# Kernel optimization log

Measured on AMD Instinct MI355X. Metric: run time of the kernel, lower is better.

The kernel has to match this reference:

```python
import jax, jax.numpy as jnp
import numpy as np

HID = 64
L = 3
RHO = 0.3
KMIN = 64
EPS = 1e-5


def conv1x1(x, w, b):
    # x: [B,C,H,W], w: [O,C], b: [O]
    return jnp.einsum('bchw,oc->bohw', x, w) + b[None, :, None, None]


def dwconv(x, w, pad, dil):
    # depthwise conv, w: [C,1,k,k], groups = C, no bias
    return jax.lax.conv_general_dilated(
        x, w, window_strides=(1, 1), padding=[(pad, pad), (pad, pad)],
        rhs_dilation=(dil, dil), feature_group_count=x.shape[1],
        dimension_numbers=('NCHW', 'OIHW', 'NCHW'))


def conv3x3(x, w, b):
    return jax.lax.conv_general_dilated(
        x, w, (1, 1), [(1, 1), (1, 1)],
        dimension_numbers=('NCHW', 'OIHW', 'NCHW')) + b[None, :, None, None]


def bn(x, g, b):
    # training-mode BatchNorm2d: batch statistics over (B,H,W) per channel
    mu = jnp.mean(x, axis=(0, 2, 3), keepdims=True)
    var = jnp.var(x, axis=(0, 2, 3), keepdims=True)
    return g[None, :, None, None] * (x - mu) * jax.lax.rsqrt(var + EPS) + b[None, :, None, None]


def setup_inputs() -> dict:
    key = jax.random.key(0)
    ks = jax.random.split(key, 40)
    B, C, H, W = 8, 1, 224, 224
    d = {}
    d['x'] = jax.random.normal(ks[0], (B, C, H, W), jnp.float32)
    # input_proj: 1x1 conv, out = 2*HID + L + 1 = 132
    d['w_in'] = jax.random.normal(ks[1], (2 * HID + L + 1, C), jnp.float32) * 0.5
    d['b_in'] = jnp.zeros((2 * HID + L + 1,), jnp.float32)
    for l in range(L):
        ksz = 2 * l + 3
        d[f'dw{l}'] = jax.random.normal(ks[2 + 4 * l], (HID, 1, ksz, ksz), jnp.float32) / ksz
        d[f'pw{l}_w'] = jax.random.normal(ks[3 + 4 * l], (HID, HID), jnp.float32) * (1.0 / np.sqrt(HID))
        d[f'pw{l}_b'] = jnp.zeros((HID,), jnp.float32)
        d[f'bn{l}_g'] = jnp.ones((HID,), jnp.float32)
        d[f'bn{l}_b'] = jnp.zeros((HID,), jnp.float32)
    d['imp_w1'] = jax.random.normal(ks[20], (HID // 4, HID), jnp.float32) * (1.0 / np.sqrt(HID))
    d['imp_b1'] = jnp.zeros((HID // 4,), jnp.float32)
    d['imp_w2'] = jax.random.normal(ks[21], (1, HID // 4, 3, 3), jnp.float32) * 0.1
    d['imp_b2'] = jnp.zeros((1,), jnp.float32)
    d['val_w'] = jax.random.normal(ks[22], (HID, HID), jnp.float32) * (1.0 / np.sqrt(HID))
    d['val_b'] = jnp.zeros((HID,), jnp.float32)
    d['out_w'] = jax.random.normal(ks[23], (HID, HID), jnp.float32) * (1.0 / np.sqrt(HID))
    d['out_b'] = jnp.zeros((HID,), jnp.float32)
    d['fin_w'] = jax.random.normal(ks[24], (HID, HID), jnp.float32) * (1.0 / np.sqrt(HID))
    d['fin_b'] = jnp.zeros((HID,), jnp.float32)
    return d


def reference(x, w_in, b_in,
              dw0, pw0_w, pw0_b, bn0_g, bn0_b,
              dw1, pw1_w, pw1_b, bn1_g, bn1_b,
              dw2, pw2_w, pw2_b, bn2_g, bn2_b,
              imp_w1, imp_b1, imp_w2, imp_b2,
              val_w, val_b, out_w, out_b, fin_w, fin_b):
    B, C, H, W = x.shape
    F_ = conv1x1(x, w_in, b_in)                       # [B, 2*HID+L+1, H, W]
    Q = F_[:, :HID]
    K = F_[:, HID:2 * HID]
    G = F_[:, 2 * HID:]                               # [B, L+1, H, W]
    # importance network: 1x1 conv -> ReLU -> 3x3 conv -> sigmoid
    imp = jax.nn.sigmoid(conv3x3(jax.nn.relu(conv1x1(K, imp_w1, imp_b1)), imp_w2, imp_b2))  # [B,1,H,W]
    # adaptive top-k sparsification: K = max(floor(rho*H*W), K_min)
    k = max(int(RHO * H * W), KMIN)
    mask_flat = imp.reshape(B, H * W)
    _, idx = jax.lax.top_k(mask_flat, k)              # [B, k]
    sparse = jnp.zeros_like(mask_flat).at[jnp.arange(B)[:, None], idx].set(1.0)
    K_cur = K * sparse.reshape(B, 1, H, W)
    # focal levels: kernel k_l = 2*l+3, dilation d_l = 2^l, pad = (k_l//2)*d_l
    levels = [(dw0, pw0_w, pw0_b, bn0_g, bn0_b, 1),
              (dw1, pw1_w, pw1_b, bn1_g, bn1_b, 2),
              (dw2, pw2_w, pw2_b, bn2_g, bn2_b, 4)]
    focal = []
    for dw, pw_w, pw_b, g, be, dil in levels:
        ksz = dw.shape[-1]
        pad = (ksz // 2) * dil
        K_cur = jax.nn.relu(bn(conv1x1(dwconv(K_cur, dw, pad, dil), pw_w, pw_b), g, be))
        focal.append(K_cur)
    Gn = jax.nn.softmax(G, axis=1)                    # softmax over L+1 gate channels
    K_agg = Gn[:, 0:1] * focal[0] + Gn[:, 1:2] * focal[1] + Gn[:, 2:3] * focal[2]
    K_global = jnp.mean(focal[-1], axis=(2, 3), keepdims=True)  # AdaptiveAvgPool2d(1), broadcast
    K_final = K_agg + Gn[:, -1:] * K_global
    V = conv1x1(K_final, val_w, val_b)
    QV = Q * V
    # output_proj Linear over channel dim (dropout is identity in eval)
    O = jnp.einsum('bchw,oc->bohw', QV, out_w) + out_b[None, :, None, None]
    # in_channels (1) != hidden_channels -> residual via final_conv on F[:, :HID] == Q
    x_proj = conv1x1(Q, fin_w, fin_b)
    return x_proj + O
```

## Files before the change

kernel.cpp:

```cpp
#include <hip/hip_runtime.h>

#define HDIM 224
#define WDIM 224
#define PPIX 50176
#define BATCH 8
#define NPIX 401408
#define KTOP 15052
#define NELEM 25690112
#define NBLK 6272
#define NBAND 14
#define NDWBLK 7168
#define NCHUNK 49

typedef __attribute__((ext_vector_type(8))) short bf8_t;
typedef __attribute__((ext_vector_type(4))) float f4_t;
typedef __attribute__((ext_vector_type(8))) unsigned short us8_t;
typedef __attribute__((ext_vector_type(4))) unsigned short us4_t;
#define MFMA_BF16 __builtin_amdgcn_mfma_f32_16x16x32_bf16

__device__ inline unsigned short f2bf(float f) {
    unsigned int u = __float_as_uint(f);
    return (unsigned short)((u + 0x7FFFu + ((u >> 16) & 1u)) >> 16);
}
__device__ inline float bf2f(unsigned short u) {
    return __uint_as_float(((unsigned int)u) << 16);
}

__device__ inline int ldsg(int r) { return ((r >> 3) ^ r) & 7; }

__device__ inline void stage_w64(const float* __restrict__ W, char* sWc, int t) {
    int o = t >> 2, cq = t & 3, c0 = cq * 16;
    const float4* src = (const float4*)(W + o * 64 + c0);
    float4 v0 = src[0], v1 = src[1], v2 = src[2], v3 = src[3];
    bf8_t p0, p1;
    p0[0] = (short)f2bf(v0.x); p0[1] = (short)f2bf(v0.y);
    p0[2] = (short)f2bf(v0.z); p0[3] = (short)f2bf(v0.w);
    p0[4] = (short)f2bf(v1.x); p0[5] = (short)f2bf(v1.y);
    p0[6] = (short)f2bf(v1.z); p0[7] = (short)f2bf(v1.w);
    p1[0] = (short)f2bf(v2.x); p1[1] = (short)f2bf(v2.y);
    p1[2] = (short)f2bf(v2.z); p1[3] = (short)f2bf(v2.w);
    p1[4] = (short)f2bf(v3.x); p1[5] = (short)f2bf(v3.y);
    p1[6] = (short)f2bf(v3.z); p1[7] = (short)f2bf(v3.w);
    int g = ldsg(o);
    *(bf8_t*)(sWc + o * 128 + (((2 * cq) ^ g) << 4)) = p0;
    *(bf8_t*)(sWc + o * 128 + (((2 * cq + 1) ^ g) << 4)) = p1;
}

__device__ inline void mfma64(const char* sWc, const char* sPc, int l, int m0, f4_t acc[4]) {
    int lr = l & 15, lg = l >> 4;
    int ra = m0 + lr, ga = ldsg(ra);
    const char* abase = sWc + ra * 128;
    bf8_t a0 = *(const bf8_t*)(abase + ((lg ^ ga) << 4));
    bf8_t a1 = *(const bf8_t*)(abase + (((lg + 4) ^ ga) << 4));
    #pragma unroll
    for (int nt = 0; nt < 4; nt++) {
        int rb = nt * 16 + lr, gb = ldsg(rb);
        const char* bbase = sPc + rb * 128;
        bf8_t b0 = *(const bf8_t*)(bbase + ((lg ^ gb) << 4));
        bf8_t b1 = *(const bf8_t*)(bbase + (((lg + 4) ^ gb) << 4));
        f4_t c = {0.f, 0.f, 0.f, 0.f};
        c = MFMA_BF16(a0, b0, c, 0, 0, 0);
        c = MFMA_BF16(a1, b1, c, 0, 0, 0);
        acc[nt] = c;
    }
}

__global__ __launch_bounds__(256) void prep_kernel(
    const float* __restrict__ w_in, const float* __restrict__ b_in,
    const float* __restrict__ imp_w1, const float* __restrict__ imp_b1,
    const float* __restrict__ fin_w, const float* __restrict__ fin_b,
    float* __restrict__ coeffs, unsigned int* __restrict__ ghist,
    unsigned int* __restrict__ pfx, int* __restrict__ rem)
{
    int t = threadIdx.x;
    if (t < 16) {
        float a = 0.f, d = 0.f;
        for (int c = 0; c < 64; c++) {
            a += imp_w1[t * 64 + c] * w_in[64 + c];
            d += imp_w1[t * 64 + c] * b_in[64 + c];
        }
        coeffs[t] = a;
        coeffs[16 + t] = d + imp_b1[t];
    }
    if (t < 64) {
        float a = 0.f, d = 0.f;
        for (int c = 0; c < 64; c++) {
            a += fin_w[t * 64 + c] * w_in[c];
            d += fin_w[t * 64 + c] * b_in[c];
        }
        coeffs[32 + t] = a;
        coeffs[96 + t] = d + fin_b[t];
    }
    for (int i = t; i < 2048; i += 256) ghist[i] = 0u;
    if (t < BATCH) { pfx[t] = 0u; rem[t] = KTOP; }
}

__global__ __launch_bounds__(256) void imp_kernel(
    const float* __restrict__ x, const float* __restrict__ coeffs,
    const float* __restrict__ imp_w2, const float* __restrict__ imp_b2,
    float* __restrict__ imp)
{
    int idx = blockIdx.x * 256 + threadIdx.x;
    int b = idx / PPIX, p = idx % PPIX;
    int h = p / WDIM, w = p % WDIM;
    float acc = imp_b2[0];
    #pragma unroll
    for (int ky = 0; ky < 3; ky++) {
        int hh = h + ky - 1;
        float okh = (hh >= 0 && hh < HDIM) ? 1.f : 0.f;
        int hc = min(max(hh, 0), HDIM - 1);
        #pragma unroll
        for (int kx = 0; kx < 3; kx++) {
            int ww = w + kx - 1;
            float ok = okh * ((ww >= 0 && ww < WDIM) ? 1.f : 0.f);
            int wc = min(max(ww, 0), WDIM - 1);
            float xv = x[b * PPIX + hc * WDIM + wc] * ok;
            #pragma unroll
            for (int c = 0; c < 16; c++) {
                float r = fmaxf(xv * coeffs[c] + coeffs[16 + c] * ok, 0.f);
                acc += r * imp_w2[c * 9 + ky * 3 + kx];
            }
        }
    }
    imp[idx] = 1.f / (1.f + expf(-acc));
}

__global__ __launch_bounds__(256) void topk_hist(
    const float* __restrict__ imp, const unsigned int* __restrict__ pfx,
    unsigned int* __restrict__ ghist, int shift)
{
    int b = blockIdx.x / NCHUNK, ch = blockIdx.x % NCHUNK;
    int t = threadIdx.x;
    __shared__ unsigned int hist[256];
    hist[t] = 0u;
    __syncthreads();
    unsigned int prefix = pfx[b];
    unsigned int himask = (shift == 24) ? 0u : (0xFFFFFFFFu << (shift + 8));
    float4 v = ((const float4*)(imp + b * PPIX + ch * 1024))[t];
    unsigned int bb[4] = {__float_as_uint(v.x), __float_as_uint(v.y),
                          __float_as_uint(v.z), __float_as_uint(v.w)};
    #pragma unroll
    for (int k = 0; k < 4; k++)
        if ((bb[k] & himask) == prefix)
            atomicAdd(&hist[(bb[k] >> shift) & 255u], 1u);
    __syncthreads();
    unsigned int c = hist[t];
    if (c) atomicAdd(&ghist[b * 256 + t], c);
}

__global__ __launch_bounds__(256) void topk_select(
    unsigned int* __restrict__ ghist, unsigned int* __restrict__ pfx,
    int* __restrict__ rem, int shift)
{
    int b = blockIdx.x;
    int t = threadIdx.x;
    __shared__ unsigned int h[256];
    h[t] = ghist[b * 256 + t];
    ghist[b * 256 + t] = 0u;
    __syncthreads();
    if (t == 0) {
        int r = rem[b];
        unsigned int bsel = 0u;
        for (int bin = 255; bin >= 0; bin--) {
            int c = (int)h[bin];
            if (c >= r) { bsel = (unsigned int)bin; break; }
            r -= c;
        }
        rem[b] = r;
        pfx[b] |= bsel << shift;
    }
}

__global__ __launch_bounds__(256) void topk_mask1(
    const float* __restrict__ imp, const unsigned int* __restrict__ pfx,
    float* __restrict__ mask, int* __restrict__ blocktie)
{
    int b = blockIdx.x / NCHUNK, ch = blockIdx.x % NCHUNK;
    int t = threadIdx.x;
    unsigned int T = pfx[b];
    float4 v = ((const float4*)(imp + b * PPIX + ch * 1024))[t];
    unsigned int bb[4] = {__float_as_uint(v.x), __float_as_uint(v.y),
                          __float_as_uint(v.z), __float_as_uint(v.w)};
    float4 mo;
    float* mp = &mo.x;
    int cnt = 0;
    #pragma unroll
    for (int k = 0; k < 4; k++) {
        mp[k] = (bb[k] > T) ? 1.f : 0.f;
        cnt += (bb[k] == T) ? 1 : 0;
    }
    ((float4*)(mask + b * PPIX + ch * 1024))[t] = mo;
    #pragma unroll
    for (int off = 32; off > 0; off >>= 1) cnt += __shfl_down(cnt, off);
    __shared__ int ws4[4];
    int lane = t & 63, wv = t >> 6;
    if (lane == 0) ws4[wv] = cnt;
    __syncthreads();
    if (t == 0) blocktie[b * NCHUNK + ch] = ws4[0] + ws4[1] + ws4[2] + ws4[3];
}

__global__ __launch_bounds__(256) void topk_mask2(
    const float* __restrict__ imp, const unsigned int* __restrict__ pfx,
    const int* __restrict__ rem_, const int* __restrict__ blocktie,
    float* __restrict__ mask)
{
    int b = blockIdx.x;
    int t = threadIdx.x, lane = t & 63, wv = t >> 6;
    unsigned int T = pfx[b];
    int rem = rem_[b];
    __shared__ int sbase[NCHUNK], scnt[NCHUNK];
    if (t == 0) {
        int s = 0;
        for (int i = 0; i < NCHUNK; i++) {
            sbase[i] = s;
            int c = blocktie[b * NCHUNK + i];
            scnt[i] = c;
            s += c;
        }
    }
    __syncthreads();
    __shared__ int wtot[4];
    for (int ch = 0; ch < NCHUNK; ch++) {
        if (scnt[ch] == 0) continue;
        int base = sbase[ch];
        if (base >= rem) break;
        for (int g = 0; g < 4; g++) {
            int i = b * PPIX + ch * 1024 + g * 256 + t;
            int flag = (__float_as_uint(imp[i]) == T) ? 1 : 0;
            unsigned long long bal = __ballot(flag);
            if (lane == 0) wtot[wv] = __popcll(bal);
            __syncthreads();
            int wbase = 0, tot = 0;
            for (int q = 0; q < 4; q++) { int c = wtot[q]; if (q < wv) wbase += c; tot += c; }
            if (flag && base + wbase + __popcll(bal & ((1ull << lane) - 1ull)) < rem)
                mask[i] = 1.f;
            base += tot;
            __syncthreads();
        }
    }
}

__global__ __launch_bounds__(256, 4) void level0_kernel(
    const float* __restrict__ x, const float* __restrict__ mask,
    const float* __restrict__ w_in, const float* __restrict__ b_in,
    const float* __restrict__ dw_w, const float* __restrict__ pw_w,
    const float* __restrict__ pw_b,
    unsigned short* __restrict__ y_out, float* __restrict__ partials)
{
    __shared__ __align__(16) short sW[4096];
    __shared__ __align__(16) short sP[4096];
    __shared__ float sred[128];
    __shared__ float sBias[64];
    char* sWc = (char*)sW; char* sPc = (char*)sP;
    int t = threadIdx.x;
    int swz = (blockIdx.x & 7) * 784 + (blockIdx.x >> 3);
    int b = swz / 784;
    int l = t & 63, og = t >> 6;
    int p0 = (swz % 784) * 64;
    int p = p0 + l;
    int h = p / WDIM, w = p % WDIM;
    stage_w64(pw_w, sWc, t);
    if (t < 64) sBias[t] = pw_b[t];

    int rowoff[3]; float okhf[3];
    int wcs[3]; float okwf[3];
    #pragma unroll
    for (int k = 0; k < 3; k++) {
        int hh = h + k - 1;
        okhf[k] = (hh >= 0 && hh < HDIM) ? 1.f : 0.f;
        rowoff[k] = min(max(hh, 0), HDIM - 1) * WDIM;
        int ww = w + k - 1;
        okwf[k] = (ww >= 0 && ww < WDIM) ? 1.f : 0.f;
        wcs[k] = min(max(ww, 0), WDIM - 1);
    }
    float mv[9], mxv[9];
    const float* mb = mask + b * PPIX;
    const float* xb = x + b * PPIX;
    #pragma unroll
    for (int ky = 0; ky < 3; ky++) {
        #pragma unroll
        for (int kx = 0; kx < 3; kx++) {
            int a = rowoff[ky] + wcs[kx];
            float mm = mb[a] * (okhf[ky] * okwf[kx]);
            mv[ky * 3 + kx] = mm;
            mxv[ky * 3 + kx] = mm * xb[a];
        }
    }
    bf8_t pk0, pk1;
    #pragma unroll
    for (int j = 0; j < 16; j++) {
        int c = og * 16 + j;
        float wk = w_in[64 + c], bk = b_in[64 + c];
        const float* dwr = dw_w + c * 9;
        float a0 = 0.f, a1 = 0.f;
        #pragma unroll
        for (int tp = 0; tp < 9; tp++) {
            float dv = dwr[tp];
            a0 += dv * mxv[tp];
            a1 += dv * mv[tp];
        }
        unsigned short bv = f2bf(wk * a0 + bk * a1);
        if (j < 8) pk0[j] = (short)bv; else pk1[j - 8] = (short)bv;
    }
    int gl = ldsg(l);
    *(bf8_t*)(sPc + l * 128 + (((2 * og) ^ gl) << 4)) = pk0;
    *(bf8_t*)(sPc + l * 128 + (((2 * og + 1) ^ gl) << 4)) = pk1;
    __syncthreads();

    int m0 = og * 16, lr = l & 15, lg = l >> 4;
    f4_t acc[4];
    mfma64(sWc, sPc, l, m0, acc);
    unsigned short* ybase = y_out + (size_t)b * 64 * PPIX + p0;
    #pragma unroll
    for (int r = 0; r < 4; r++) {
        int o = m0 + 4 * lg + r;
        float bias = sBias[o];
        float s = 0.f, s2 = 0.f;
        #pragma unroll
        for (int nt = 0; nt < 4; nt++) {
            float yv = acc[nt][r] + bias;
            ybase[(size_t)o * PPIX + nt * 16 + lr] = f2bf(yv);
            s += yv; s2 += yv * yv;
        }
        #pragma unroll
        for (int m = 1; m < 16; m <<= 1) {
            s += __shfl_xor(s, m);
            s2 += __shfl_xor(s2, m);
        }
        if (lr == 0) { sred[2 * o] = s; sred[2 * o + 1] = s2; }
    }
    __syncthreads();
    if (t < 128) partials[(size_t)blockIdx.x * 128 + t] = sred[t];
}

template<int KSZ, int DIL>
__global__ __launch_bounds__(256, 3) void dw_kernel(
    const unsigned short* __restrict__ in, const float* __restrict__ bnp,
    const float* __restrict__ dw_w, unsigned short* __restrict__ out)
{
    constexpr int PAD = (KSZ / 2) * DIL;
    constexpr int BH = 16;
    constexpr int LR = BH + 2 * PAD;
    constexpr int SW = WDIM + 2 * PAD + 4;
    constexpr int SEG = 16 + 2 * PAD;
    __shared__ float sIn[LR * SW];

    int t = threadIdx.x;
    int swz = (blockIdx.x & 7) * (NDWBLK / 8) + (blockIdx.x >> 3);
    int bc = swz / NBAND, band = swz % NBAND;
    int c = bc & 63;
    int r0 = band * BH;
    float sc = bnp[c], sh = bnp[64 + c];
    const unsigned short* plane = in + (size_t)bc * PPIX;

    constexpr int PADC = SW - WDIM;
    for (int i = t; i < LR * PADC; i += 256) {
        int r = i / PADC, cc = i % PADC;
        int col = (cc < PAD) ? cc : (cc + WDIM);
        sIn[r * SW + col] = 0.f;
    }
    for (int i = t; i < LR * 28; i += 256) {
        int sr = i / 28, q = i % 28;
        int gr = r0 - PAD + sr;
        float4 a = {0.f, 0.f, 0.f, 0.f}, bq = {0.f, 0.f, 0.f, 0.f};
        if (gr >= 0 && gr < HDIM) {
            us8_t v = *(const us8_t*)(plane + gr * WDIM + 8 * q);
            a.x = fmaxf(sc * bf2f(v[0]) + sh, 0.f);
            a.y = fmaxf(sc * bf2f(v[1]) + sh, 0.f);
            a.z = fmaxf(sc * bf2f(v[2]) + sh, 0.f);
            a.w = fmaxf(sc * bf2f(v[3]) + sh, 0.f);
            bq.x = fmaxf(sc * bf2f(v[4]) + sh, 0.f);
            bq.y = fmaxf(sc * bf2f(v[5]) + sh, 0.f);
            bq.z = fmaxf(sc * bf2f(v[6]) + sh, 0.f);
            bq.w = fmaxf(sc * bf2f(v[7]) + sh, 0.f);
        }
        *(float4*)(sIn + sr * SW + PAD + 8 * q) = a;
        *(float4*)(sIn + sr * SW + PAD + 8 * q + 4) = bq;
    }
    __syncthreads();

    if (t < 224) {
        const float* dwr = dw_w + c * KSZ * KSZ;
        float wk[KSZ * KSZ];
        #pragma unroll
        for (int i = 0; i < KSZ * KSZ; i++) wk[i] = dwr[i];

        int xs = t % 14, row = t / 14;
        int x0 = xs * 16;
        float acc[16];
        #pragma unroll
        for (int j = 0; j < 16; j++) acc[j] = 0.f;
        #pragma unroll
        for (int ky = 0; ky < KSZ; ky++) {
            const float4* srow = (const float4*)(sIn + (row + ky * DIL) * SW + x0);
            float s[SEG];
            #pragma unroll
            for (int i = 0; i < SEG / 4; i++) ((float4*)s)[i] = srow[i];
            #pragma unroll
            for (int kx = 0; kx < KSZ; kx++) {
                float wv = wk[ky * KSZ + kx];
                #pragma unroll
                for (int j = 0; j < 16; j++)
                    acc[j] += s[j + DIL * kx] * wv;
            }
        }
        us8_t o0, o1;
        #pragma unroll
        for (int j = 0; j < 8; j++) { o0[j] = f2bf(acc[j]); o1[j] = f2bf(acc[8 + j]); }
        unsigned short* orow = out + (size_t)bc * PPIX + (r0 + row) * WDIM + x0;
        *(us8_t*)orow = o0;
        *(us8_t*)(orow + 8) = o1;
    }
}

__global__ __launch_bounds__(256, 4) void pw_kernel(
    const float* __restrict__ pw_w, const float* __restrict__ pw_b,
    const unsigned short* __restrict__ src_y, unsigned short* __restrict__ dst_y,
    float* __restrict__ partials)
{
    __shared__ __align__(16) short sW[4096];
    __shared__ __align__(16) short sP[4096];
    __shared__ float sred[128];
    __shared__ float sBias[64];
    char* sWc = (char*)sW; char* sPc = (char*)sP;
    int t = threadIdx.x;
    int swz = (blockIdx.x & 7) * 784 + (blockIdx.x >> 3);
    int b = swz / 784;
    int p0 = (swz % 784) * 64;
    stage_w64(pw_w, sWc, t);
    if (t < 64) sBias[t] = pw_b[t];

    const unsigned short* sbase_g = src_y + (size_t)b * 64 * PPIX + p0;
    unsigned short* dbase_g = dst_y + (size_t)b * 64 * PPIX + p0;
    {
        int c = t >> 2, pg = t & 3;
        const unsigned short* src = sbase_g + (size_t)c * PPIX + 16 * pg;
        us8_t v0 = *(const us8_t*)src;
        us8_t v1 = *(const us8_t*)(src + 8);
        int kc = c >> 3, cb = 2 * (c & 7);
        #pragma unroll
        for (int e = 0; e < 16; e++) {
            int r = 16 * pg + e;
            int gr = ldsg(r);
            unsigned short val = (e < 8) ? (unsigned short)v0[e] : (unsigned short)v1[e - 8];
            *(unsigned short*)(sPc + r * 128 + ((kc ^ gr) << 4) + cb) = val;
        }
    }
    __syncthreads();

    int l = t & 63, wv = t >> 6, m0 = wv * 16;
    int lr = l & 15, lg = l >> 4;
    f4_t acc[4];
    mfma64(sWc, sPc, l, m0, acc);
    #pragma unroll
    for (int r = 0; r < 4; r++) {
        int o = m0 + 4 * lg + r;
        float bias = sBias[o];
        float s = 0.f, s2 = 0.f;
        #pragma unroll
        for (int nt = 0; nt < 4; nt++) {
            float yv = acc[nt][r] + bias;
            dbase_g[(size_t)o * PPIX + nt * 16 + lr] = f2bf(yv);
            s += yv; s2 += yv * yv;
        }
        #pragma unroll
        for (int m = 1; m < 16; m <<= 1) {
            s += __shfl_xor(s, m);
            s2 += __shfl_xor(s2, m);
        }
        if (lr == 0) { sred[2 * o] = s; sred[2 * o + 1] = s2; }
    }
    __syncthreads();
    if (t < 128) partials[(size_t)blockIdx.x * 128 + t] = sred[t];
}

__global__ __launch_bounds__(256) void bnfin_kernel(
    const float* __restrict__ partials,
    const float* __restrict__ g, const float* __restrict__ be,
    float* __restrict__ bnp)
{
    int c = blockIdx.x;
    int t = threadIdx.x;
    float s = 0.f, s2 = 0.f;
    for (int blk = t; blk < NBLK; blk += 256) {
        s  += partials[(size_t)blk * 128 + 2 * c];
        s2 += partials[(size_t)blk * 128 + 2 * c + 1];
    }
    #pragma unroll
    for (int off = 32; off > 0; off >>= 1) {
        s += __shfl_down(s, off);
        s2 += __shfl_down(s2, off);
    }
    __shared__ float wsm[8];
    int lane = t & 63, wv = t >> 6;
    if (lane == 0) { wsm[wv] = s; wsm[4 + wv] = s2; }
    __syncthreads();
    if (t == 0) {
        s = wsm[0] + wsm[1] + wsm[2] + wsm[3];
        s2 = wsm[4] + wsm[5] + wsm[6] + wsm[7];
        const float inv_n = 1.f / (float)NPIX;
        float mu = s * inv_n;
        float var = s2 * inv_n - mu * mu;
        float sc = g[c] * rsqrtf(var + 1e-5f);
        bnp[c] = sc;
        bnp[64 + c] = be[c] - mu * sc;
    }
}

__global__ __launch_bounds__(256) void kglobal_kernel(
    const unsigned short* __restrict__ y2, const float* __restrict__ bnp2,
    float* __restrict__ kg)
{
    int bc = blockIdx.x;
    int c = bc & 63;
    int t = threadIdx.x;
    const unsigned short* row = y2 + (size_t)bc * PPIX;
    float sc = bnp2[c], sh = bnp2[64 + c];
    float s = 0.f;
    for (int ii = t; ii < PPIX / 8; ii += 256) {
        us8_t v = *(const us8_t*)(row + 8 * ii);
        #pragma unroll
        for (int k = 0; k < 8; k++) s += fmaxf(sc * bf2f(v[k]) + sh, 0.f);
    }
    #pragma unroll
    for (int off = 32; off > 0; off >>= 1) s += __shfl_down(s, off);
    __shared__ float wsum[4];
    int lane = t & 63, wv = t >> 6;
    if (lane == 0) wsum[wv] = s;
    __syncthreads();
    if (t == 0) kg[bc] = (wsum[0] + wsum[1] + wsum[2] + wsum[3]) * (1.f / (float)PPIX);
}

__global__ __launch_bounds__(256, 4) void final_kernel(
    const float* __restrict__ x, const float* __restrict__ w_in,
    const float* __restrict__ b_in,
    const unsigned short* __restrict__ y0, const unsigned short* __restrict__ y1,
    const unsigned short* __restrict__ y2,
    const float* __restrict__ bnp, const float* __restrict__ kg,
    const float* __restrict__ val_w, const float* __restrict__ val_b,
    const float* __restrict__ out_w, const float* __restrict__ out_b,
    const float* __restrict__ coeffs, float* __restrict__ out)
{
    __shared__ __align__(16) short sVW[4096];
    __shared__ __align__(16) short sOW[4096];
    __shared__ __align__(16) short sP[4096];
    __shared__ float sxv[64], sQW[64], sQB[64], sVB[64], sOB[64], sC1[64], sC2[64];
    char* sVWc = (char*)sVW; char* sOWc = (char*)sOW; char* sPc = (char*)sP;
    int t = threadIdx.x;
    int blk = blockIdx.x;
    int b = blk / 784;
    int l = t & 63, wv = t >> 6;
    int p0 = (blk % 784) * 64;
    stage_w64(val_w, sVWc, t);
    stage_w64(out_w, sOWc, t);
    if (t < 64) {
        sQW[t] = w_in[t]; sQB[t] = b_in[t];
        sVB[t] = val_b[t]; sOB[t] = out_b[t];
        sC1[t] = coeffs[32 + t]; sC2[t] = coeffs[96 + t];
    }

    float xv = x[b * PPIX + p0 + l];
    if (wv == 0) sxv[l] = xv;
    float g0 = xv * w_in[128] + b_in[128];
    float g1 = xv * w_in[129] + b_in[129];
    float g2 = xv * w_in[130] + b_in[130];
    float g3 = xv * w_in[131] + b_in[131];
    float mx = fmaxf(fmaxf(g0, g1), fmaxf(g2, g3));
    float e0 = expf(g0 - mx), e1 = expf(g1 - mx), e2 = expf(g2 - mx), e3 = expf(g3 - mx);
    float inv = 1.f / (e0 + e1 + e2 + e3);
    float G0 = e0 * inv, G1 = e1 * inv, G2 = e2 * inv, G3 = e3 * inv;

    bf8_t pk0, pk1;
    #pragma unroll
    for (int j = 0; j < 16; j++) {
        int c = wv * 16 + j;
        size_t idx = (size_t)(b * 64 + c) * PPIX + p0 + l;
        float f0 = fmaxf(bnp[c] * bf2f(y0[idx]) + bnp[64 + c], 0.f);
        float f1 = fmaxf(bnp[128 + c] * bf2f(y1[idx]) + bnp[192 + c], 0.f);
        float f2 = fmaxf(bnp[256 + c] * bf2f(y2[idx]) + bnp[320 + c], 0.f);
        float kf = G0 * f0 + G1 * f1 + G2 * f2 + G3 * kg[b * 64 + c];
        unsigned short bv = f2bf(kf);
        if (j < 8) pk0[j] = (short)bv; else pk1[j - 8] = (short)bv;
    }
    int gl = ldsg(l);
    *(bf8_t*)(sPc + l * 128 + (((2 * wv) ^ gl) << 4)) = pk0;
    *(bf8_t*)(sPc + l * 128 + (((2 * wv + 1) ^ gl) << 4)) = pk1;
    __syncthreads();

    int m0 = wv * 16, lr = l & 15, lg = l >> 4;
    f4_t accV[4];
    mfma64(sVWc, sPc, l, m0, accV);
    __syncthreads();

    #pragma unroll
    for (int nt = 0; nt < 4; nt++) {
        float xvp = sxv[nt * 16 + lr];
        us4_t q4;
        #pragma unroll
        for (int r = 0; r < 4; r++) {
            int o = m0 + 4 * lg + r;
            float V = accV[nt][r] + sVB[o];
            float q = xvp * sQW[o] + sQB[o];
            q4[r] = f2bf(q * V);
        }
        int rb = nt * 16 + lr, gb = ldsg(rb);
        int kc = 2 * wv + (lg >> 1);
        *(us4_t*)(sPc + rb * 128 + ((kc ^ gb) << 4) + 8 * (lg & 1)) = q4;
    }
    __syncthreads();

    f4_t accO[4];
    mfma64(sOWc, sPc, l, m0, accO);
    #pragma unroll
    for (int nt = 0; nt < 4; nt++) {
        float xvp = sxv[nt * 16 + lr];
        #pragma unroll
        for (int r = 0; r < 4; r++) {
            int o = m0 + 4 * lg + r;
            out[(size_t)(b * 64 + o) * PPIX + p0 + nt * 16 + lr] =
                accO[nt][r] + sOB[o] + xvp * sC1[o] + sC2[o];
        }
    }
}

extern "C" void kernel_launch(void* const* d_in, const int* in_sizes, int n_in,
                              void* d_out, int out_size, void* d_ws, size_t ws_size,
                              hipStream_t stream)
{
    (void)in_sizes; (void)n_in; (void)out_size; (void)ws_size;
    const float* x      = (const float*)d_in[0];
    const float* w_in   = (const float*)d_in[1];
    const float* b_in   = (const float*)d_in[2];
    const float* dw0    = (const float*)d_in[3];
    const float* pw0_w  = (const float*)d_in[4];
    const float* pw0_b  = (const float*)d_in[5];
    const float* bn0_g  = (const float*)d_in[6];
    const float* bn0_b  = (const float*)d_in[7];
    const float* dw1    = (const float*)d_in[8];
    const float* pw1_w  = (const float*)d_in[9];
    const float* pw1_b  = (const float*)d_in[10];
    const float* bn1_g  = (const float*)d_in[11];
    const float* bn1_b  = (const float*)d_in[12];
    const float* dw2    = (const float*)d_in[13];
    const float* pw2_w  = (const float*)d_in[14];
    const float* pw2_b  = (const float*)d_in[15];
    const float* bn2_g  = (const float*)d_in[16];
    const float* bn2_b  = (const float*)d_in[17];
    const float* imp_w1 = (const float*)d_in[18];
    const float* imp_b1 = (const float*)d_in[19];
    const float* imp_w2 = (const float*)d_in[20];
    const float* imp_b2 = (const float*)d_in[21];
    const float* val_w  = (const float*)d_in[22];
    const float* val_b  = (const float*)d_in[23];
    const float* out_w  = (const float*)d_in[24];
    const float* out_b  = (const float*)d_in[25];
    const float* fin_w  = (const float*)d_in[26];
    const float* fin_b  = (const float*)d_in[27];

    unsigned short* y0 = (unsigned short*)d_ws;
    unsigned short* y1 = y0 + (size_t)NELEM;
    unsigned short* y2 = y1 + (size_t)NELEM;
    unsigned short* yt = y2 + (size_t)NELEM;
    float* imp  = (float*)(yt + (size_t)NELEM);
    float* mask = imp + NPIX;
    float* partials = mask + NPIX;
    float* bnp   = partials + (size_t)NBLK * 128;
    float* kg    = bnp + 384;
    float* coeffs = kg + 512;
    unsigned int* ghist = (unsigned int*)(coeffs + 160);
    unsigned int* pfx   = ghist + 2048;
    int* rem            = (int*)(pfx + 8);
    int* blocktie       = rem + 8;
    float* outp = (float*)d_out;

    prep_kernel<<<1, 256, 0, stream>>>(w_in, b_in, imp_w1, imp_b1, fin_w, fin_b,
                                       coeffs, ghist, pfx, rem);
    imp_kernel<<<NPIX / 256, 256, 0, stream>>>(x, coeffs, imp_w2, imp_b2, imp);

    for (int shift = 24; shift >= 0; shift -= 8) {
        topk_hist<<<BATCH * NCHUNK, 256, 0, stream>>>(imp, pfx, ghist, shift);
        topk_select<<<BATCH, 256, 0, stream>>>(ghist, pfx, rem, shift);
    }
    topk_mask1<<<BATCH * NCHUNK, 256, 0, stream>>>(imp, pfx, mask, blocktie);
    topk_mask2<<<BATCH, 256, 0, stream>>>(imp, pfx, rem, blocktie, mask);

    level0_kernel<<<NBLK, 256, 0, stream>>>(x, mask, w_in, b_in, dw0, pw0_w, pw0_b,
                                            y0, partials);
    bnfin_kernel<<<64, 256, 0, stream>>>(partials, bn0_g, bn0_b, bnp);

    dw_kernel<5, 2><<<NDWBLK, 256, 0, stream>>>(y0, bnp, dw1, yt);
    pw_kernel<<<NBLK, 256, 0, stream>>>(pw1_w, pw1_b, yt, y1, partials);
    bnfin_kernel<<<64, 256, 0, stream>>>(partials, bn1_g, bn1_b, bnp + 128);

    dw_kernel<7, 4><<<NDWBLK, 256, 0, stream>>>(y1, bnp + 128, dw2, yt);
    pw_kernel<<<NBLK, 256, 0, stream>>>(pw2_w, pw2_b, yt, y2, partials);
    bnfin_kernel<<<64, 256, 0, stream>>>(partials, bn2_g, bn2_b, bnp + 256);

    kglobal_kernel<<<512, 256, 0, stream>>>(y2, bnp + 256, kg);
    final_kernel<<<NBLK, 256, 0, stream>>>(x, w_in, b_in, y0, y1, y2, bnp, kg,
                                           val_w, val_b, out_w, out_b, coeffs, outp);
}
```

Measured before the change: 391.6 us.

## Fuse top-k select into histogram pass, parallelize tie fix, raise occupancy bounds

The top-k radix select now runs the bin choice inside the histogram kernel, using a last-block-done atomic counter, so the separate select launches go away. The mask and tie resolution is split into a per-chunk budget computed by the last block and a parallel tie-fix kernel, replacing the serial single-block-per-batch loop. Separately, launch-bounds occupancy hints are raised on the level0, pw, dw and final kernels, and kglobal uses 1024-thread blocks. The higher occupancy hints may force register spills, and the done counters add atomic and fence traffic.

```diff
diff --git a/kernel.cpp b/kernel.cpp
--- a/kernel.cpp
+++ b/kernel.cpp
@@ -70,7 +70,8 @@
     const float* __restrict__ imp_w1, const float* __restrict__ imp_b1,
     const float* __restrict__ fin_w, const float* __restrict__ fin_b,
     float* __restrict__ coeffs, unsigned int* __restrict__ ghist,
-    unsigned int* __restrict__ pfx, int* __restrict__ rem)
+    unsigned int* __restrict__ pfx, int* __restrict__ rem,
+    unsigned int* __restrict__ done)
 {
     int t = threadIdx.x;
     if (t < 16) {
@@ -92,6 +93,7 @@
         coeffs[96 + t] = d + fin_b[t];
     }
     for (int i = t; i < 2048; i += 256) ghist[i] = 0u;
+    if (t < 48) done[t] = 0u;
     if (t < BATCH) { pfx[t] = 0u; rem[t] = KTOP; }
 }
 
@@ -125,13 +127,15 @@
     imp[idx] = 1.f / (1.f + expf(-acc));
 }
 
-__global__ __launch_bounds__(256) void topk_hist(
-    const float* __restrict__ imp, const unsigned int* __restrict__ pfx,
-    unsigned int* __restrict__ ghist, int shift)
+__global__ __launch_bounds__(256) void topk_histsel(
+    const float* __restrict__ imp, unsigned int* __restrict__ pfx,
+    int* __restrict__ rem, unsigned int* __restrict__ ghist,
+    unsigned int* __restrict__ done_pass, int shift)
 {
     int b = blockIdx.x / NCHUNK, ch = blockIdx.x % NCHUNK;
     int t = threadIdx.x;
     __shared__ unsigned int hist[256];
+    __shared__ unsigned int tk;
     hist[t] = 0u;
     __syncthreads();
     unsigned int prefix = pfx[b];
@@ -146,34 +150,34 @@
     __syncthreads();
     unsigned int c = hist[t];
     if (c) atomicAdd(&ghist[b * 256 + t], c);
-}
-
-__global__ __launch_bounds__(256) void topk_select(
-    unsigned int* __restrict__ ghist, unsigned int* __restrict__ pfx,
-    int* __restrict__ rem, int shift)
-{
-    int b = blockIdx.x;
-    int t = threadIdx.x;
-    __shared__ unsigned int h[256];
-    h[t] = ghist[b * 256 + t];
-    ghist[b * 256 + t] = 0u;
     __syncthreads();
     if (t == 0) {
-        int r = rem[b];
-        unsigned int bsel = 0u;
-        for (int bin = 255; bin >= 0; bin--) {
-            int c = (int)h[bin];
-            if (c >= r) { bsel = (unsigned int)bin; break; }
-            r -= c;
-        }
-        rem[b] = r;
-        pfx[b] |= bsel << shift;
-    }
-}
-
-__global__ __launch_bounds__(256) void topk_mask1(
+        __threadfence();
+        tk = atomicAdd(&done_pass[b], 1u);
+    }
+    __syncthreads();
+    if (tk == NCHUNK - 1) {
+        unsigned int cnt = atomicExch(&ghist[b * 256 + t], 0u);
+        hist[t] = cnt;
+        __syncthreads();
+        if (t == 0) {
+            int r = rem[b];
+            unsigned int bsel = 0u;
+            for (int bin = 255; bin >= 0; bin--) {
+                int cc = (int)hist[bin];
+                if (cc >= r) { bsel = (unsigned int)bin; break; }
+                r -= cc;
+            }
+            rem[b] = r;
+            pfx[b] |= bsel << shift;
+        }
+    }
+}
+
+__global__ __launch_bounds__(256) void topk_mask(
     const float* __restrict__ imp, const unsigned int* __restrict__ pfx,
-    float* __restrict__ mask, int* __restrict__ blocktie)
+    const int* __restrict__ rem, float* __restrict__ mask,
+    unsigned int* __restrict__ blocktie, unsigned int* __restrict__ done_m)
 {
     int b = blockIdx.x / NCHUNK, ch = blockIdx.x % NCHUNK;
     int t = threadIdx.x;
@@ -193,54 +197,55 @@
     #pragma unroll
     for (int off = 32; off > 0; off >>= 1) cnt += __shfl_down(cnt, off);
     __shared__ int ws4[4];
+    __shared__ unsigned int tk;
     int lane = t & 63, wv = t >> 6;
     if (lane == 0) ws4[wv] = cnt;
     __syncthreads();
-    if (t == 0) blocktie[b * NCHUNK + ch] = ws4[0] + ws4[1] + ws4[2] + ws4[3];
-}
-
-__global__ __launch_bounds__(256) void topk_mask2(
+    if (t == 0) {
+        atomicExch(&blocktie[b * NCHUNK + ch],
+                   (unsigned int)(ws4[0] + ws4[1] + ws4[2] + ws4[3]));
+        __threadfence();
+        tk = atomicAdd(&done_m[b], 1u);
+    }
+    __syncthreads();
+    if (tk == NCHUNK - 1 && t == 0) {
+        int base = 0, r = rem[b];
+        for (int i = 0; i < NCHUNK; i++) {
+            int ci = (int)atomicAdd(&blocktie[b * NCHUNK + i], 0u);
+            int budget = min(max(r - base, 0), ci);
+            base += ci;
+            atomicExch(&blocktie[b * NCHUNK + i], (unsigned int)budget);
+        }
+    }
+}
+
+__global__ __launch_bounds__(256) void topk_tiefix(
     const float* __restrict__ imp, const unsigned int* __restrict__ pfx,
-    const int* __restrict__ rem_, const int* __restrict__ blocktie,
-    float* __restrict__ mask)
-{
-    int b = blockIdx.x;
+    const unsigned int* __restrict__ blocktie, float* __restrict__ mask)
+{
+    int b = blockIdx.x / NCHUNK, ch = blockIdx.x % NCHUNK;
+    int budget = (int)blocktie[b * NCHUNK + ch];
+    if (budget == 0) return;
     int t = threadIdx.x, lane = t & 63, wv = t >> 6;
     unsigned int T = pfx[b];
-    int rem = rem_[b];
-    __shared__ int sbase[NCHUNK], scnt[NCHUNK];
-    if (t == 0) {
-        int s = 0;
-        for (int i = 0; i < NCHUNK; i++) {
-            sbase[i] = s;
-            int c = blocktie[b * NCHUNK + i];
-            scnt[i] = c;
-            s += c;
-        }
-    }
-    __syncthreads();
     __shared__ int wtot[4];
-    for (int ch = 0; ch < NCHUNK; ch++) {
-        if (scnt[ch] == 0) continue;
-        int base = sbase[ch];
-        if (base >= rem) break;
-        for (int g = 0; g < 4; g++) {
-            int i = b * PPIX + ch * 1024 + g * 256 + t;
-            int flag = (__float_as_uint(imp[i]) == T) ? 1 : 0;
-            unsigned long long bal = __ballot(flag);
-            if (lane == 0) wtot[wv] = __popcll(bal);
-            __syncthreads();
-            int wbase = 0, tot = 0;
-            for (int q = 0; q < 4; q++) { int c = wtot[q]; if (q < wv) wbase += c; tot += c; }
-            if (flag && base + wbase + __popcll(bal & ((1ull << lane) - 1ull)) < rem)
-                mask[i] = 1.f;
-            base += tot;
-            __syncthreads();
-        }
-    }
-}
-
-__global__ __launch_bounds__(256, 4) void level0_kernel(
+    int base = 0;
+    for (int g = 0; g < 4; g++) {
+        int i = b * PPIX + ch * 1024 + g * 256 + t;
+        int flag = (__float_as_uint(imp[i]) == T) ? 1 : 0;
+        unsigned long long bal = __ballot(flag);
+        if (lane == 0) wtot[wv] = __popcll(bal);
+        __syncthreads();
+        int wbase = 0, tot = 0;
+        for (int q = 0; q < 4; q++) { int c = wtot[q]; if (q < wv) wbase += c; tot += c; }
+        if (flag && base + wbase + __popcll(bal & ((1ull << lane) - 1ull)) < budget)
+            mask[i] = 1.f;
+        base += tot;
+        __syncthreads();
+    }
+}
+
+__global__ __launch_bounds__(256, 6) void level0_kernel(
     const float* __restrict__ x, const float* __restrict__ mask,
     const float* __restrict__ w_in, const float* __restrict__ b_in,
     const float* __restrict__ dw_w, const float* __restrict__ pw_w,
@@ -333,8 +338,8 @@
     if (t < 128) partials[(size_t)blockIdx.x * 128 + t] = sred[t];
 }
 
-template<int KSZ, int DIL>
-__global__ __launch_bounds__(256, 3) void dw_kernel(
+template<int KSZ, int DIL, int OCC>
+__global__ __launch_bounds__(256, OCC) void dw_kernel(
     const unsigned short* __restrict__ in, const float* __restrict__ bnp,
     const float* __restrict__ dw_w, unsigned short* __restrict__ out)
 {
@@ -413,7 +418,7 @@
     }
 }
 
-__global__ __launch_bounds__(256, 4) void pw_kernel(
+__global__ __launch_bounds__(256, 6) void pw_kernel(
     const float* __restrict__ pw_w, const float* __restrict__ pw_b,
     const unsigned short* __restrict__ src_y, unsigned short* __restrict__ dst_y,
     float* __restrict__ partials)
@@ -507,7 +512,7 @@
     }
 }
 
-__global__ __launch_bounds__(256) void kglobal_kernel(
+__global__ __launch_bounds__(1024) void kglobal_kernel(
     const unsigned short* __restrict__ y2, const float* __restrict__ bnp2,
     float* __restrict__ kg)
 {
@@ -517,21 +522,26 @@
     const unsigned short* row = y2 + (size_t)bc * PPIX;
     float sc = bnp2[c], sh = bnp2[64 + c];
     float s = 0.f;
-    for (int ii = t; ii < PPIX / 8; ii += 256) {
+    for (int ii = t; ii < PPIX / 8; ii += 1024) {
         us8_t v = *(const us8_t*)(row + 8 * ii);
         #pragma unroll
         for (int k = 0; k < 8; k++) s += fmaxf(sc * bf2f(v[k]) + sh, 0.f);
     }
     #pragma unroll
     for (int off = 32; off > 0; off >>= 1) s += __shfl_down(s, off);
-    __shared__ float wsum[4];
+    __shared__ float wsum[16];
     int lane = t & 63, wv = t >> 6;
     if (lane == 0) wsum[wv] = s;
     __syncthreads();
-    if (t == 0) kg[bc] = (wsum[0] + wsum[1] + wsum[2] + wsum[3]) * (1.f / (float)PPIX);
-}
-
-__global__ __launch_bounds__(256, 4) void final_kernel(
+    if (t == 0) {
+        float tot = 0.f;
+        #pragma unroll
+        for (int q = 0; q < 16; q++) tot += wsum[q];
+        kg[bc] = tot * (1.f / (float)PPIX);
+    }
+}
+
+__global__ __launch_bounds__(256, 6) void final_kernel(
     const float* __restrict__ x, const float* __restrict__ w_in,
     const float* __restrict__ b_in,
     const unsigned short* __restrict__ y0, const unsigned short* __restrict__ y1,
@@ -670,33 +680,35 @@
     unsigned int* ghist = (unsigned int*)(coeffs + 160);
     unsigned int* pfx   = ghist + 2048;
     int* rem            = (int*)(pfx + 8);
-    int* blocktie       = rem + 8;
+    unsigned int* blocktie = (unsigned int*)(rem + 8);
+    unsigned int* done  = blocktie + 8 * NCHUNK;
     float* outp = (float*)d_out;
 
     prep_kernel<<<1, 256, 0, stream>>>(w_in, b_in, imp_w1, imp_b1, fin_w, fin_b,
-                                       coeffs, ghist, pfx, rem);
+                                       coeffs, ghist, pfx, rem, done);
     imp_kernel<<<NPIX / 256, 256, 0, stream>>>(x, coeffs, imp_w2, imp_b2, imp);
 
-    for (int shift = 24; shift >= 0; shift -= 8) {
-        topk_hist<<<BATCH * NCHUNK, 256, 0, stream>>>(imp, pfx, ghist, shift);
-        topk_select<<<BATCH, 256, 0, stream>>>(ghist, pfx, rem, shift);
-    }
-    topk_mask1<<<BATCH * NCHUNK, 256, 0, stream>>>(imp, pfx, mask, blocktie);
-    topk_mask2<<<BATCH, 256, 0, stream>>>(imp, pfx, rem, blocktie, mask);
+    for (int pass = 0; pass < 4; pass++) {
+        topk_histsel<<<BATCH * NCHUNK, 256, 0, stream>>>(
+            imp, pfx, rem, ghist, done + pass * 8, 24 - 8 * pass);
+    }
+    topk_mask<<<BATCH * NCHUNK, 256, 0, stream>>>(imp, pfx, rem, mask, blocktie,
+                                                  done + 32);
+    topk_tiefix<<<BATCH * NCHUNK, 256, 0, stream>>>(imp, pfx, blocktie, mask);
 
     level0_kernel<<<NBLK, 256, 0, stream>>>(x, mask, w_in, b_in, dw0, pw0_w, pw0_b,
                                             y0, partials);
     bnfin_kernel<<<64, 256, 0, stream>>>(partials, bn0_g, bn0_b, bnp);
 
-    dw_kernel<5, 2><<<NDWBLK, 256, 0, stream>>>(y0, bnp, dw1, yt);
+    dw_kernel<5, 2, 6><<<NDWBLK, 256, 0, stream>>>(y0, bnp, dw1, yt);
     pw_kernel<<<NBLK, 256, 0, stream>>>(pw1_w, pw1_b, yt, y1, partials);
     bnfin_kernel<<<64, 256, 0, stream>>>(partials, bn1_g, bn1_b, bnp + 128);
 
-    dw_kernel<7, 4><<<NDWBLK, 256, 0, stream>>>(y1, bnp + 128, dw2, yt);
+    dw_kernel<7, 4, 4><<<NDWBLK, 256, 0, stream>>>(y1, bnp + 128, dw2, yt);
     pw_kernel<<<NBLK, 256, 0, stream>>>(pw2_w, pw2_b, yt, y2, partials);
     bnfin_kernel<<<64, 256, 0, stream>>>(partials, bn2_g, bn2_b, bnp + 256);
 
-    kglobal_kernel<<<512, 256, 0, stream>>>(y2, bnp + 256, kg);
+    kglobal_kernel<<<512, 1024, 0, stream>>>(y2, bnp + 256, kg);
     final_kernel<<<NBLK, 256, 0, stream>>>(x, w_in, b_in, y0, y1, y2, bnp, kg,
                                            val_w, val_b, out_w, out_b, coeffs, outp);
 }
```

Result: slower. 453.7 us (+15.9%).
